# Optimization experiments

Hardware: AMD Instinct MI355X
Metric: run time of the kernel (lower is better)

## Reference

```python
import jax, jax.numpy as jnp
import numpy as np

NUM_LABELS = 10  # number of distinct label values in the minibatch
EPS = 1e-8


def setup_inputs() -> dict:
    key = jax.random.key(0)
    k1, k2 = jax.random.split(key)
    z = jax.random.normal(k1, (8192, 20, 256), dtype=jnp.float32)  # [B, C, H]
    labels = jax.random.randint(k2, (8192,), 0, NUM_LABELS)  # [B]
    return {"z": z, "labels": labels}


def reference(z, labels):
    # CODI minibatch loss, positive pairs, representation space.
    # Equivalent to: for each unique label, mse(z[group] + 1e-8, mean(z[group]))
    # summed over labels. Vectorized as a single segment-mean +
    # gather-broadcast + segment-SSE pass (one traversal of z).
    z = jnp.nan_to_num(z)
    B, C, H = z.shape
    counts = jax.ops.segment_sum(
        jnp.ones((B,), dtype=z.dtype), labels, num_segments=NUM_LABELS
    )  # [K]
    sums = jax.ops.segment_sum(z, labels, num_segments=NUM_LABELS)  # [K, C, H]
    means = jnp.nan_to_num(sums / jnp.maximum(counts, 1.0)[:, None, None])
    # per-sample squared distance to its group's mean (note the +EPS as in torch)
    d = (z + EPS) - means[labels]  # [B, C, H]
    per_sample = jnp.sum(d * d, axis=(1, 2))  # [B]
    sse = jax.ops.segment_sum(per_sample, labels, num_segments=NUM_LABELS)  # [K]
    # nn.MSELoss is a mean over all elements of the group: count_k * C * H
    mse_k = sse / (jnp.maximum(counts, 1.0) * (C * H))
    # torch.unique only visits labels present in the batch -> mask empty groups
    return jnp.sum(jnp.where(counts > 0, jnp.nan_to_num(mse_k), 0.0))
```

## Files before the change

### kernel.cpp

```cpp
#include <hip/hip_runtime.h>

#define B_SZ   8192
#define CH     5120
#define CH4    1280
#define K_LAB  10
#define EPS    1e-8f
#define FLTMAX 3.402823466e38f

#define NTHR   320
#define PS     64
#define RB     3


__global__ __launch_bounds__(640) void codi_setup(
    const int* __restrict__ labels, int* __restrict__ idx,
    int* __restrict__ off, float* __restrict__ SSQ, float* __restrict__ nsq)
{
    __shared__ int lab_s[B_SZ];
    __shared__ int cnts[K_LAB];
    __shared__ int offs[K_LAB + 1];
    const int tid  = threadIdx.x;
    const int k    = tid >> 6;
    const int lane = tid & 63;

    const int4* l4 = (const int4*)labels;
    for (int i = tid; i < B_SZ / 4; i += 640) ((int4*)lab_s)[i] = l4[i];
    __syncthreads();

    int cnt = 0;
    for (int b0 = 0; b0 < B_SZ; b0 += 64)
        cnt += __popcll(__ballot(lab_s[b0 + lane] == k));
    if (lane == 0) cnts[k] = cnt;
    __syncthreads();
    if (tid == 0) {
        int a = 0;
        for (int j = 0; j < K_LAB; ++j) { offs[j] = a; a += cnts[j]; }
        offs[K_LAB] = a;
    }
    __syncthreads();

    int base = offs[k];
    const unsigned long long ltmask = (1ULL << lane) - 1ULL;
    for (int b0 = 0; b0 < B_SZ; b0 += 64) {
        int lab = lab_s[b0 + lane];
        unsigned long long m = __ballot(lab == k);
        if (lab == k) idx[base + __popcll(m & ltmask)] = b0 + lane;
        base += __popcll(m);
    }
    if (tid < K_LAB + 1) off[tid] = offs[tid];
    if (tid < K_LAB) { SSQ[tid] = 0.f; nsq[tid] = 0.f; }
}

__global__ __launch_bounds__(NTHR) void codi_gather(
    const float4* __restrict__ z4, const int* __restrict__ idx,
    const int* __restrict__ off, float4* __restrict__ S_part,
    float* __restrict__ SSQ)
{
    const int tid = threadIdx.x;
    const int k   = blockIdx.x / PS;
    const int ps  = blockIdx.x % PS;

    const int kb  = off[k];
    const int cnt = off[k + 1] - kb;
    const int s0  = kb + (int)(((long long)cnt * ps) / PS);
    const int s1  = kb + (int)(((long long)cnt * (ps + 1)) / PS);
    const int n   = s1 - s0;

    __shared__ int rows[160];
    for (int i = tid; i < n; i += NTHR) rows[i] = idx[s0 + i];
    __syncthreads();

    float4 sum[4];
    #pragma unroll
    for (int j = 0; j < 4; ++j) sum[j] = make_float4(0.f, 0.f, 0.f, 0.f);
    float ssq = 0.f;

#define SANITIZE(v) do { \
        v.x = (v.x == v.x) ? fminf(fmaxf(v.x, -FLTMAX), FLTMAX) : 0.f; \
        v.y = (v.y == v.y) ? fminf(fmaxf(v.y, -FLTMAX), FLTMAX) : 0.f; \
        v.z = (v.z == v.z) ? fminf(fmaxf(v.z, -FLTMAX), FLTMAX) : 0.f; \
        v.w = (v.w == v.w) ? fminf(fmaxf(v.w, -FLTMAX), FLTMAX) : 0.f; \
    } while (0)
#define ACCUM(j, v) do { \
        sum[j].x += v.x; sum[j].y += v.y; sum[j].z += v.z; sum[j].w += v.w; \
        ssq = fmaf(v.x, v.x, ssq); ssq = fmaf(v.y, v.y, ssq); \
        ssq = fmaf(v.z, v.z, ssq); ssq = fmaf(v.w, v.w, ssq); \
    } while (0)

    const int n_main = n - (n % RB);
    for (int i0 = 0; i0 < n_main; i0 += RB) {
        float4 vb[RB][4];
        #pragma unroll
        for (int u = 0; u < RB; ++u) {
            const size_t rbase = (size_t)rows[i0 + u] * CH4;
            #pragma unroll
            for (int j = 0; j < 4; ++j)
                vb[u][j] = z4[rbase + j * NTHR + tid];
        }
        #pragma unroll
        for (int u = 0; u < RB; ++u)
            #pragma unroll
            for (int j = 0; j < 4; ++j) { SANITIZE(vb[u][j]); ACCUM(j, vb[u][j]); }
    }
    for (int i = n_main; i < n; ++i) {
        const size_t rbase = (size_t)rows[i] * CH4;
        float4 vb[4];
        #pragma unroll
        for (int j = 0; j < 4; ++j) vb[j] = z4[rbase + j * NTHR + tid];
        #pragma unroll
        for (int j = 0; j < 4; ++j) { SANITIZE(vb[j]); ACCUM(j, vb[j]); }
    }
#undef SANITIZE
#undef ACCUM

    float4* sp = S_part + (size_t)blockIdx.x * CH4;
    #pragma unroll
    for (int j = 0; j < 4; ++j) sp[j * NTHR + tid] = sum[j];

    #pragma unroll
    for (int o = 32; o > 0; o >>= 1) ssq += __shfl_down(ssq, o, 64);
    if ((tid & 63) == 0) atomicAdd(&SSQ[k], ssq);
}

__global__ __launch_bounds__(NTHR) void codi_reduce(
    const float4* __restrict__ S_part, float* __restrict__ nsq)
{
    const int tid = threadIdx.x;
    const int k   = blockIdx.x >> 2;
    const int cc  = blockIdx.x & 3;
    float4 s = make_float4(0.f, 0.f, 0.f, 0.f);
    #pragma unroll 8
    for (int ps = 0; ps < PS; ++ps) {
        float4 v = S_part[((size_t)(k * PS + ps)) * CH4 + cc * NTHR + tid];
        s.x += v.x; s.y += v.y; s.z += v.z; s.w += v.w;
    }
    float w = fmaf(s.x, s.x, fmaf(s.y, s.y, fmaf(s.z, s.z, s.w * s.w)));
    #pragma unroll
    for (int o = 32; o > 0; o >>= 1) w += __shfl_down(w, o, 64);
    if ((tid & 63) == 0) atomicAdd(&nsq[k], w);
}

__global__ __launch_bounds__(64) void codi_final(
    const int* __restrict__ off, const float* __restrict__ SSQ,
    const float* __restrict__ nsq, float* __restrict__ out)
{
    if (threadIdx.x == 0) {
        float loss = 0.f;
        for (int k = 0; k < K_LAB; ++k) {
            float n = (float)(off[k + 1] - off[k]);
            if (n > 0.f) {
                float sse = SSQ[k] - nsq[k] / n + n * (float)CH * (EPS * EPS);
                float mse = sse / (n * (float)CH);
                if (mse == mse) loss += mse;
            }
        }
        out[0] = loss;
    }
}

extern "C" void kernel_launch(void* const* d_in, const int* in_sizes, int n_in,
                              void* d_out, int out_size, void* d_ws, size_t ws_size,
                              hipStream_t stream) {
    const float4* z4     = (const float4*)d_in[0];
    const int*    labels = (const int*)d_in[1];

    float* hdr    = (float*)d_ws;
    float* SSQ    = hdr;
    float* nsq    = hdr + 16;
    int*   off    = (int*)(hdr + 32);
    int*   idx    = (int*)(hdr + 64);
    float* S_part = hdr + 64 + B_SZ;

    codi_setup<<<1, 640, 0, stream>>>(labels, idx, off, SSQ, nsq);
    codi_gather<<<K_LAB * PS, NTHR, 0, stream>>>(
        z4, idx, off, (float4*)S_part, SSQ);
    codi_reduce<<<K_LAB * 4, NTHR, 0, stream>>>((const float4*)S_part, nsq);
    codi_final<<<1, 64, 0, stream>>>(off, SSQ, nsq, (float*)d_out);
}
```

Before: 279.1 us.

## Double-buffer row loads in gather and fold final kernel into reduce

```diff
diff --git a/kernel.cpp b/kernel.cpp
--- a/kernel.cpp
+++ b/kernel.cpp
@@ -9,12 +9,13 @@
 
 #define NTHR   320
 #define PS     64
-#define RB     3
+#define ST     2
 
 
 __global__ __launch_bounds__(640) void codi_setup(
     const int* __restrict__ labels, int* __restrict__ idx,
-    int* __restrict__ off, float* __restrict__ SSQ, float* __restrict__ nsq)
+    int* __restrict__ off, float* __restrict__ SSQ, float* __restrict__ nsq,
+    int* __restrict__ done)
 {
     __shared__ int lab_s[B_SZ];
     __shared__ int cnts[K_LAB];
@@ -49,6 +50,7 @@
     }
     if (tid < K_LAB + 1) off[tid] = offs[tid];
     if (tid < K_LAB) { SSQ[tid] = 0.f; nsq[tid] = 0.f; }
+    if (tid == 0) *done = 0;
 }
 
 __global__ __launch_bounds__(NTHR) void codi_gather(
@@ -75,43 +77,52 @@
     for (int j = 0; j < 4; ++j) sum[j] = make_float4(0.f, 0.f, 0.f, 0.f);
     float ssq = 0.f;
 
-#define SANITIZE(v) do { \
-        v.x = (v.x == v.x) ? fminf(fmaxf(v.x, -FLTMAX), FLTMAX) : 0.f; \
-        v.y = (v.y == v.y) ? fminf(fmaxf(v.y, -FLTMAX), FLTMAX) : 0.f; \
-        v.z = (v.z == v.z) ? fminf(fmaxf(v.z, -FLTMAX), FLTMAX) : 0.f; \
-        v.w = (v.w == v.w) ? fminf(fmaxf(v.w, -FLTMAX), FLTMAX) : 0.f; \
-    } while (0)
-#define ACCUM(j, v) do { \
-        sum[j].x += v.x; sum[j].y += v.y; sum[j].z += v.z; sum[j].w += v.w; \
-        ssq = fmaf(v.x, v.x, ssq); ssq = fmaf(v.y, v.y, ssq); \
-        ssq = fmaf(v.z, v.z, ssq); ssq = fmaf(v.w, v.w, ssq); \
-    } while (0)
+#define ISSUE(BUF, W, S_) do { \
+        _Pragma("unroll") \
+        for (int u = 0; u < ST; ++u) { \
+            int i_ = (S_) * ST + u; \
+            int ic_ = (i_ < n) ? i_ : n - 1; \
+            W[u] = (i_ < n) ? 1.f : 0.f; \
+            const size_t rb_ = (size_t)rows[ic_] * CH4; \
+            _Pragma("unroll") \
+            for (int j = 0; j < 4; ++j) BUF[u][j] = z4[rb_ + j * NTHR + tid]; \
+        } } while (0)
 
-    const int n_main = n - (n % RB);
-    for (int i0 = 0; i0 < n_main; i0 += RB) {
-        float4 vb[RB][4];
-        #pragma unroll
-        for (int u = 0; u < RB; ++u) {
-            const size_t rbase = (size_t)rows[i0 + u] * CH4;
-            #pragma unroll
-            for (int j = 0; j < 4; ++j)
-                vb[u][j] = z4[rbase + j * NTHR + tid];
+#define CONSUME(BUF, W) do { \
+        _Pragma("unroll") \
+        for (int u = 0; u < ST; ++u) { \
+            _Pragma("unroll") \
+            for (int j = 0; j < 4; ++j) { \
+                float4 v = BUF[u][j]; \
+                v.x = (v.x == v.x) ? fminf(fmaxf(v.x, -FLTMAX), FLTMAX) : 0.f; \
+                v.y = (v.y == v.y) ? fminf(fmaxf(v.y, -FLTMAX), FLTMAX) : 0.f; \
+                v.z = (v.z == v.z) ? fminf(fmaxf(v.z, -FLTMAX), FLTMAX) : 0.f; \
+                v.w = (v.w == v.w) ? fminf(fmaxf(v.w, -FLTMAX), FLTMAX) : 0.f; \
+                v.x *= W[u]; v.y *= W[u]; v.z *= W[u]; v.w *= W[u]; \
+                sum[j].x += v.x; sum[j].y += v.y; \
+                sum[j].z += v.z; sum[j].w += v.w; \
+                ssq = fmaf(v.x, v.x, ssq); ssq = fmaf(v.y, v.y, ssq); \
+                ssq = fmaf(v.z, v.z, ssq); ssq = fmaf(v.w, v.w, ssq); \
+            } \
+        } } while (0)
+
+    if (n > 0) {
+        const int nst = (n + ST - 1) / ST;
+        float4 A[ST][4], B[ST][4];
+        float  wa[ST], wb[ST];
+        ISSUE(A, wa, 0);
+        int s = 0;
+        while (s + 1 < nst) {
+            ISSUE(B, wb, s + 1);
+            CONSUME(A, wa);
+            if (s + 2 < nst) ISSUE(A, wa, s + 2);
+            CONSUME(B, wb);
+            s += 2;
         }
-        #pragma unroll
-        for (int u = 0; u < RB; ++u)
-            #pragma unroll
-            for (int j = 0; j < 4; ++j) { SANITIZE(vb[u][j]); ACCUM(j, vb[u][j]); }
+        if (s < nst) CONSUME(A, wa);
     }
-    for (int i = n_main; i < n; ++i) {
-        const size_t rbase = (size_t)rows[i] * CH4;
-        float4 vb[4];
-        #pragma unroll
-        for (int j = 0; j < 4; ++j) vb[j] = z4[rbase + j * NTHR + tid];
-        #pragma unroll
-        for (int j = 0; j < 4; ++j) { SANITIZE(vb[j]); ACCUM(j, vb[j]); }
-    }
-#undef SANITIZE
-#undef ACCUM
+#undef ISSUE
+#undef CONSUME
 
     float4* sp = S_part + (size_t)blockIdx.x * CH4;
     #pragma unroll
@@ -123,11 +134,15 @@
 }
 
 __global__ __launch_bounds__(NTHR) void codi_reduce(
-    const float4* __restrict__ S_part, float* __restrict__ nsq)
+    const float4* __restrict__ S_part, float* __restrict__ nsq,
+    const float* __restrict__ SSQ, const int* __restrict__ off,
+    int* __restrict__ done, float* __restrict__ out)
 {
     const int tid = threadIdx.x;
     const int k   = blockIdx.x >> 2;
     const int cc  = blockIdx.x & 3;
+    __shared__ float wsum[5];
+
     float4 s = make_float4(0.f, 0.f, 0.f, 0.f);
     #pragma unroll 8
     for (int ps = 0; ps < PS; ++ps) {
@@ -137,24 +152,26 @@
     float w = fmaf(s.x, s.x, fmaf(s.y, s.y, fmaf(s.z, s.z, s.w * s.w)));
     #pragma unroll
     for (int o = 32; o > 0; o >>= 1) w += __shfl_down(w, o, 64);
-    if ((tid & 63) == 0) atomicAdd(&nsq[k], w);
-}
+    if ((tid & 63) == 0) wsum[tid >> 6] = w;
+    __syncthreads();
 
-__global__ __launch_bounds__(64) void codi_final(
-    const int* __restrict__ off, const float* __restrict__ SSQ,
-    const float* __restrict__ nsq, float* __restrict__ out)
-{
-    if (threadIdx.x == 0) {
-        float loss = 0.f;
-        for (int k = 0; k < K_LAB; ++k) {
-            float n = (float)(off[k + 1] - off[k]);
-            if (n > 0.f) {
-                float sse = SSQ[k] - nsq[k] / n + n * (float)CH * (EPS * EPS);
-                float mse = sse / (n * (float)CH);
-                if (mse == mse) loss += mse;
+    if (tid == 0) {
+        atomicAdd(&nsq[k], wsum[0] + wsum[1] + wsum[2] + wsum[3] + wsum[4]);
+        __threadfence();
+        int t = atomicAdd(done, 1);
+        if (t == K_LAB * 4 - 1) {
+            float loss = 0.f;
+            for (int kk = 0; kk < K_LAB; ++kk) {
+                float nn = (float)(off[kk + 1] - off[kk]);
+                if (nn > 0.f) {
+                    float ns  = atomicAdd(&nsq[kk], 0.f);
+                    float sse = SSQ[kk] - ns / nn + nn * (float)CH * (EPS * EPS);
+                    float mse = sse / (nn * (float)CH);
+                    if (mse == mse) loss += mse;
+                }
             }
+            out[0] = loss;
         }
-        out[0] = loss;
     }
 }
 
@@ -168,12 +185,13 @@
     float* SSQ    = hdr;
     float* nsq    = hdr + 16;
     int*   off    = (int*)(hdr + 32);
+    int*   done   = (int*)(hdr + 48);
     int*   idx    = (int*)(hdr + 64);
     float* S_part = hdr + 64 + B_SZ;
 
-    codi_setup<<<1, 640, 0, stream>>>(labels, idx, off, SSQ, nsq);
+    codi_setup<<<1, 640, 0, stream>>>(labels, idx, off, SSQ, nsq, done);
     codi_gather<<<K_LAB * PS, NTHR, 0, stream>>>(
         z4, idx, off, (float4*)S_part, SSQ);
-    codi_reduce<<<K_LAB * 4, NTHR, 0, stream>>>((const float4*)S_part, nsq);
-    codi_final<<<1, 64, 0, stream>>>(off, SSQ, nsq, (float*)d_out);
+    codi_reduce<<<K_LAB * 4, NTHR, 0, stream>>>(
+        (const float4*)S_part, nsq, SSQ, off, done, (float*)d_out);
 }
```

Measured after the change: 268.6 us. 3.8% less time.
